# Kernel optimization log

Measured on AMD Instinct MI355X. Metric: run time of the kernel, lower is better.

## Reference

```python
import jax, jax.numpy as jnp
import numpy as np
from jax import lax

CL, IL = 128, 64            # context_length, inst_length (globals in original)
PC, CH1, CH2, CH3 = 64, 128, 256, 256
CK1 = CK2 = CK3 = 3
F1, OUT = 400, 1
B = 4096
C3_OUT = CH3 * (CL - 1 - CK1 - CK2 - CK3 + 3)   # 256*121 = 30976
F1_IN = C3_OUT + CL * IL                        # 39168


def _uni(k, shape, fan_in):
    s = 1.0 / np.sqrt(fan_in)
    return jax.random.uniform(k, shape, jnp.float32, -s, s)


def setup_inputs() -> dict:
    key = jax.random.key(0)
    ks = jax.random.split(key, 14)
    x = jax.random.normal(ks[0], (B, CL * IL), jnp.float32)
    Wp = _uni(ks[1], (PC, IL, 2), IL * 2); bp = _uni(ks[2], (PC,), IL * 2)
    W1 = _uni(ks[3], (CH1, PC, CK1), PC * CK1); b1 = _uni(ks[4], (CH1,), PC * CK1)
    W2 = _uni(ks[5], (CH2, CH1, CK2), CH1 * CK2); b2 = _uni(ks[6], (CH2,), CH1 * CK2)
    W3 = _uni(ks[7], (CH3, CH2, CK3), CH2 * CK3); b3 = _uni(ks[8], (CH3,), CH2 * CK3)
    Wf1 = _uni(ks[9], (F1, F1_IN), F1_IN); bf1 = _uni(ks[10], (F1,), F1_IN)
    Wf2 = _uni(ks[11], (OUT, F1), F1); bf2 = _uni(ks[12], (OUT,), F1)
    return dict(x=x, Wp=Wp, bp=bp, W1=W1, b1=b1, W2=W2, b2=b2,
                W3=W3, b3=b3, Wf1=Wf1, bf1=bf1, Wf2=Wf2, bf2=bf2)


def _conv1d(h, w, b):
    # h: [B,C,L], w: [O,C,K], valid conv, stride 1
    return lax.conv_general_dilated(h, w, (1,), 'VALID',
                                    dimension_numbers=('NCH', 'OIH', 'NCH')) + b[None, :, None]


def reference(x, Wp, bp, W1, b1, W2, b2, W3, b3, Wf1, bf1, Wf2, bf2):
    b = x.shape[0]
    xt = x.reshape(b, CL, IL).transpose(0, 2, 1)          # [B, IL, CL]
    # Fused pairwise convp: original loops i=1..CL-1 over k=2 Conv1d on
    # (x[:,:,0], x[:,:,i]); equivalent to one shared term + one batched matmul.
    base = jnp.einsum('pc,bc->bp', Wp[:, :, 0], xt[:, :, 0])        # [B, PC]
    rest = jnp.einsum('pc,bci->bpi', Wp[:, :, 1], xt[:, :, 1:])     # [B, PC, CL-1]
    h = jax.nn.relu(base[:, :, None] + rest + bp[None, :, None])
    h = jax.nn.relu(_conv1d(h, W1, b1))
    h = jax.nn.relu(_conv1d(h, W2, b2))
    h = jax.nn.relu(_conv1d(h, W3, b3))
    h = h.reshape(b, C3_OUT)
    h = jnp.concatenate([h, xt.reshape(b, IL * CL)], axis=1)        # [B, F1_IN]
    h = jax.nn.relu(h @ Wf1.T + bf1)
    return h @ Wf2.T + bf2
```

## Files before the change

### kernel.cpp

```cpp
#include <hip/hip_runtime.h>


typedef __attribute__((ext_vector_type(8))) short bf16x8;
typedef __attribute__((ext_vector_type(4))) float f32x4;
typedef __attribute__((ext_vector_type(8))) unsigned short u16x8;
typedef __attribute__((ext_vector_type(4))) unsigned short u16x4;

#define DEVINL __device__ __forceinline__

DEVINL unsigned short f2bf(float f) {
  unsigned u = __builtin_bit_cast(unsigned, f);
  return (unsigned short)((u + 0x7fffu + ((u >> 16) & 1u)) >> 16);
}
DEVINL float bf2f(unsigned short h) {
  return __builtin_bit_cast(float, ((unsigned)h) << 16);
}
DEVINL f32x4 mfma16(bf16x8 a, bf16x8 b, f32x4 c) {
  return __builtin_amdgcn_mfma_f32_16x16x32_bf16(a, b, c, 0, 0, 0);
}
DEVINL float relu(float v) { return v > 0.f ? v : 0.f; }
DEVINL int sxg(int r, int c, int sh) {
  return (r << sh) + (((c >> 3) ^ (r & 7)) << 3) + (c & 7);
}

constexpr int NB = 4096;

__global__ __launch_bounds__(256) void k_prep_w(
    const float* __restrict__ Wp, const float* __restrict__ W1,
    const float* __restrict__ W2, const float* __restrict__ W3,
    unsigned short* __restrict__ wp1r, unsigned short* __restrict__ w1p,
    unsigned short* __restrict__ w2p, unsigned short* __restrict__ w3p) {
  int idx = blockIdx.x * 256 + threadIdx.x;
  if (idx < 4096) {
    int p = idx >> 6, i = idx & 63;
    wp1r[idx] = f2bf(Wp[(p * 64 + i) * 2 + 1]);
    return;
  }
  idx -= 4096;
  if (idx < 24576) {
    int f = idx >> 9, l = (idx >> 3) & 63, e = idx & 7;
    int mt = f & 7, t = f >> 3, ks = t & 1, k = t >> 1;
    int o = mt * 16 + (l & 15), c = ks * 32 + (l >> 4) * 8 + e;
    w1p[idx] = f2bf(W1[(o * 64 + c) * 3 + k]);
    return;
  }
  idx -= 24576;
  if (idx < 98304) {
    int f = idx >> 9, l = (idx >> 3) & 63, e = idx & 7;
    int mt = f & 15, t = f >> 4, ks = t & 3, k = t >> 2;
    int o = mt * 16 + (l & 15), c = ks * 32 + (l >> 4) * 8 + e;
    w2p[idx] = f2bf(W2[(o * 128 + c) * 3 + k]);
    return;
  }
  idx -= 98304;
  if (idx < 196608) {
    int f = idx >> 9, l = (idx >> 3) & 63, e = idx & 7;
    int mt = f & 15, t = f >> 4, ks = t & 7, k = t >> 3;
    int o = mt * 16 + (l & 15), c = ks * 32 + (l >> 4) * 8 + e;
    w3p[idx] = f2bf(W3[(o * 256 + c) * 3 + k]);
  }
}

__global__ __launch_bounds__(256) void k_prep_wf1(const float* __restrict__ wf1,
                                                  unsigned short* __restrict__ wf1r) {
  extern __shared__ unsigned short tls[];
  const int m = blockIdx.x, tid = threadIdx.x;
  const float* src = wf1 + (size_t)m * 39168;
  unsigned short* dst = wf1r + (size_t)m * 39168;
  for (int idx = tid; idx < 30976; idx += 256) {
    int o = idx / 121, l = idx - o * 121;
    tls[o * 130 + l] = f2bf(src[idx]);
  }
  __syncthreads();
  for (int idx = tid; idx < 30976; idx += 256) {
    int l = idx >> 8, o = idx & 255;
    dst[idx] = tls[o * 130 + l];
  }
  __syncthreads();
  for (int idx = tid; idx < 8192; idx += 256) {
    int il = idx >> 7, cl = idx & 127;
    tls[cl * 66 + il] = f2bf(src[30976 + idx]);
  }
  __syncthreads();
  for (int idx = tid; idx < 8192; idx += 256) {
    int cl = idx >> 6, il = idx & 63;
    dst[30976 + idx] = tls[cl * 66 + il];
  }
}

template <int CIN, int COUT, int LIN, int LOUT, int SSHI, int SSHO, bool TOGLB>
DEVINL void conv16(const unsigned short* in_lds,
                   const unsigned short* __restrict__ wpack,
                   const float* __restrict__ bias, unsigned short* out_lds,
                   unsigned short* h3, int b, int lane, int wv) {
  constexpr int KS = CIN / 32;
  constexpr int MT = COUT / 16;
  constexpr int MPW = MT / 4;
  const int lr = lane & 15, lq = lane >> 4;
  const int wm = wv >> 1, wn = wv & 1;
  f32x4 acc[MPW][4];
#pragma unroll
  for (int mi = 0; mi < MPW; ++mi)
#pragma unroll
    for (int ni = 0; ni < 4; ++ni) acc[mi][ni] = (f32x4){0.f, 0.f, 0.f, 0.f};
#pragma unroll
  for (int k = 0; k < 3; ++k)
#pragma unroll
    for (int ks = 0; ks < KS; ++ks) {
      bf16x8 a[MPW];
#pragma unroll
      for (int mi = 0; mi < MPW; ++mi)
        a[mi] = *(const bf16x8*)(wpack +
                                 (((k * KS + ks) * MT + wm * MPW + mi) << 9) +
                                 lane * 8);
      const int col = ks * 32 + lq * 8;
#pragma unroll
      for (int ni = 0; ni < 4; ++ni) {
        int l = (wn * 4 + ni) * 16 + lr + k;
        if (l > LIN - 1) l = LIN - 1;
        bf16x8 bb = *(const bf16x8*)(in_lds + sxg(l, col, SSHI));
#pragma unroll
        for (int mi = 0; mi < MPW; ++mi) acc[mi][ni] = mfma16(a[mi], bb, acc[mi][ni]);
      }
    }
#pragma unroll
  for (int mi = 0; mi < MPW; ++mi) {
    const int o0 = (wm * MPW + mi) * 16 + lq * 4;
    const f32x4 bi = *(const f32x4*)(bias + o0);
#pragma unroll
    for (int ni = 0; ni < 4; ++ni) {
      const int l = (wn * 4 + ni) * 16 + lr;
      if (l < LOUT) {
        u16x4 pk;
#pragma unroll
        for (int r = 0; r < 4; ++r) pk[r] = f2bf(relu(acc[mi][ni][r] + bi[r]));
        if constexpr (TOGLB)
          *(u16x4*)(h3 + ((size_t)b * LOUT + l) * COUT + o0) = pk;
        else
          *(u16x4*)(out_lds + sxg(l, o0, SSHO)) = pk;
      }
    }
  }
}

__global__ __launch_bounds__(512) void k_front(
    const float* __restrict__ x, const float* __restrict__ Wp,
    const float* __restrict__ bp, const unsigned short* __restrict__ wp1r,
    const unsigned short* __restrict__ w1p, const float* __restrict__ b1,
    const unsigned short* __restrict__ w2p, const float* __restrict__ b2,
    const unsigned short* __restrict__ w3p, const float* __restrict__ b3,
    unsigned short* __restrict__ h3) {
  extern __shared__ unsigned short lds[];
  unsigned short* xs = lds;
  unsigned short* h1s = lds;
  unsigned short* h0s = lds + 16000;
  unsigned short* h2s = lds + 16000;
  __shared__ float pbase[8][64];
  __shared__ float basel[64];
  const int b = blockIdx.x, tid = threadIdx.x;
  const int lane = tid & 63, wv = tid >> 6, lq = lane >> 4, lr = lane & 15;
  const float* xb = x + (size_t)b * 8192;

  for (int idx = tid * 4; idx < 8192; idx += 2048) {
    f32x4 v = *(const f32x4*)(xb + idx);
    int c = idx >> 6, i = idx & 63;
    u16x4 pk;
#pragma unroll
    for (int r = 0; r < 4; ++r) pk[r] = f2bf(v[r]);
    *(u16x4*)(xs + sxg(c, i, 6)) = pk;
  }
  __syncthreads();

  {
    int p = tid & 63, q = tid >> 6;
    float s = 0.f;
#pragma unroll
    for (int t = 0; t < 8; ++t) {
      int i = q * 8 + t;
      s += Wp[(p * 64 + i) * 2] * bf2f(xs[i]);
    }
    pbase[q][p] = s;
  }
  __syncthreads();
  if (tid < 64) {
    float s = bp[tid];
#pragma unroll
    for (int q = 0; q < 8; ++q) s += pbase[q][tid];
    basel[tid] = s;
  }
  __syncthreads();

  {
    const int mt = wv & 3, nh = wv >> 2;
    f32x4 acc[4];
#pragma unroll
    for (int t = 0; t < 4; ++t) acc[t] = (f32x4){0.f, 0.f, 0.f, 0.f};
#pragma unroll
    for (int s = 0; s < 2; ++s) {
      bf16x8 a = *(const bf16x8*)(wp1r + (mt * 16 + lr) * 64 + s * 32 + lq * 8);
#pragma unroll
      for (int t = 0; t < 4; ++t) {
        int j = (nh * 4 + t) * 16 + lr;
        int row = j + 1 > 127 ? 127 : j + 1;
        bf16x8 bb = *(const bf16x8*)(xs + sxg(row, s * 32 + lq * 8, 6));
        acc[t] = mfma16(a, bb, acc[t]);
      }
    }
    const int m0 = mt * 16 + lq * 4;
    f32x4 bl;
#pragma unroll
    for (int r = 0; r < 4; ++r) bl[r] = basel[m0 + r];
#pragma unroll
    for (int t = 0; t < 4; ++t) {
      int j = (nh * 4 + t) * 16 + lr;
      if (j < 127) {
        u16x4 pk;
#pragma unroll
        for (int r = 0; r < 4; ++r) pk[r] = f2bf(relu(acc[t][r] + bl[r]));
        *(u16x4*)(h0s + sxg(j, m0, 6)) = pk;
      }
    }
  }
  __syncthreads();

  conv16<64, 128, 127, 125, 6, 7, false>(h0s, w1p, b1, h1s, nullptr, b, lane, wv);
  __syncthreads();
  conv16<128, 256, 125, 123, 7, 8, false>(h1s, w2p, b2, h2s, nullptr, b, lane, wv);
  __syncthreads();
  conv16<256, 256, 123, 121, 8, 0, true>(h2s, w3p, b3, nullptr, h3, b, lane, wv);
}

__global__ __launch_bounds__(512) void k_fc1(const unsigned short* __restrict__ h3,
                                             const float* __restrict__ x,
                                             const unsigned short* __restrict__ wf1r,
                                             float* __restrict__ fpart, int chunkN) {
  __shared__ unsigned short lB[128 * 64];
  const int tid = threadIdx.x;
  const int lane = tid & 63, wv = tid >> 6, lq = lane >> 4, lr = lane & 15;
  const int slice = blockIdx.x & 31;
  const int bbase = (blockIdx.x >> 5) * 128;
  const int c0 = slice * 19 + (slice < 4 ? slice : 4);
  const int c1 = c0 + 19 + (slice < 4 ? 1 : 0);

  f32x4 acc[3][8], acc24;
#pragma unroll
  for (int mi = 0; mi < 3; ++mi)
#pragma unroll
    for (int nt = 0; nt < 8; ++nt) acc[mi][nt] = (f32x4){0.f, 0.f, 0.f, 0.f};
  acc24 = (f32x4){0.f, 0.f, 0.f, 0.f};

  const size_t arow0 = (size_t)((3 * wv + 0) * 16 + lr) * 39168;
  const size_t arow1 = (size_t)((3 * wv + 1) * 16 + lr) * 39168;
  const size_t arow2 = (size_t)((3 * wv + 2) * 16 + lr) * 39168;
  const size_t arow24 = (size_t)(384 + lr) * 39168;

  for (int kc = c0; kc < c1; ++kc) {
    const int k0 = kc * 64;
#pragma unroll
    for (int t = 0; t < 2; ++t) {
      int idx = tid + t * 512;
      int n = idx >> 3, ch = idx & 7;
      int bb = bbase + n;
      u16x8 v;
      if (k0 < 30976) {
        v = *(const u16x8*)(h3 + (size_t)bb * 30976 + k0 + ch * 8);
      } else {
        const float* sxp = x + (size_t)bb * 8192 + (k0 - 30976) + ch * 8;
        f32x4 v0 = *(const f32x4*)sxp;
        f32x4 v1 = *(const f32x4*)(sxp + 4);
#pragma unroll
        for (int r = 0; r < 4; ++r) {
          v[r] = f2bf(v0[r]);
          v[4 + r] = f2bf(v1[r]);
        }
      }
      *(u16x8*)(lB + (n << 6) + ((ch ^ (n & 7)) << 3)) = v;
    }
    __syncthreads();

#pragma unroll
    for (int win = 0; win < 2; ++win) {
      const int koff = k0 + win * 32 + lq * 8;
      bf16x8 a0 = *(const bf16x8*)(wf1r + arow0 + koff);
      bf16x8 a1 = *(const bf16x8*)(wf1r + arow1 + koff);
      bf16x8 a2 = *(const bf16x8*)(wf1r + arow2 + koff);
      bf16x8 a24 = *(const bf16x8*)(wf1r + arow24 + koff);
      const int cloc = win * 32 + lq * 8;
#pragma unroll
      for (int nt = 0; nt < 8; ++nt) {
        const int n = nt * 16 + lr;
        bf16x8 bb = *(const bf16x8*)(lB + sxg(n, cloc, 6));
        acc[0][nt] = mfma16(a0, bb, acc[0][nt]);
        acc[1][nt] = mfma16(a1, bb, acc[1][nt]);
        acc[2][nt] = mfma16(a2, bb, acc[2][nt]);
      }
      {
        const int n = wv * 16 + lr;
        bf16x8 bb = *(const bf16x8*)(lB + sxg(n, cloc, 6));
        acc24 = mfma16(a24, bb, acc24);
      }
    }
    __syncthreads();
  }

#pragma unroll
  for (int mi = 0; mi < 3; ++mi) {
    const int m0 = (3 * wv + mi) * 16 + lq * 4;
#pragma unroll
    for (int nt = 0; nt < 8; ++nt) {
      const int bb = bbase + nt * 16 + lr;
      *(f32x4*)(fpart + ((size_t)slice * chunkN + bb) * 400 + m0) = acc[mi][nt];
    }
  }
  {
    const int bb = bbase + wv * 16 + lr;
    *(f32x4*)(fpart + ((size_t)slice * chunkN + bb) * 400 + 384 + lq * 4) = acc24;
  }
}

__global__ __launch_bounds__(256) void k_fc1red(const float* __restrict__ fpart,
                                                const float* __restrict__ bf1,
                                                float* __restrict__ fc, int chunkN) {
  int idx = blockIdx.x * 256 + threadIdx.x;
  if (idx >= chunkN * 400) return;
  int m = idx % 400;
  float s = bf1[m];
  size_t stride = (size_t)chunkN * 400;
#pragma unroll 8
  for (int sl = 0; sl < 32; ++sl) s += fpart[(size_t)sl * stride + idx];
  fc[idx] = relu(s);
}

__global__ __launch_bounds__(256) void k_fc2(const float* __restrict__ fc,
                                             const float* __restrict__ wf2,
                                             const float* __restrict__ bf2,
                                             float* __restrict__ out) {
  int b = blockIdx.x * 4 + (threadIdx.x >> 6);
  int lane = threadIdx.x & 63;
  float s = 0.f;
  for (int m = lane; m < 400; m += 64) s += fc[(size_t)b * 400 + m] * wf2[m];
#pragma unroll
  for (int off = 32; off > 0; off >>= 1) s += __shfl_down(s, off, 64);
  if (lane == 0) out[b] = s + bf2[0];
}

extern "C" void kernel_launch(void* const* d_in, const int* in_sizes, int n_in,
                              void* d_out, int out_size, void* d_ws, size_t ws_size,
                              hipStream_t stream) {
  const float* x = (const float*)d_in[0];
  const float* Wp = (const float*)d_in[1];
  const float* bp = (const float*)d_in[2];
  const float* W1 = (const float*)d_in[3];
  const float* b1 = (const float*)d_in[4];
  const float* W2 = (const float*)d_in[5];
  const float* b2 = (const float*)d_in[6];
  const float* W3 = (const float*)d_in[7];
  const float* b3 = (const float*)d_in[8];
  const float* Wf1 = (const float*)d_in[9];
  const float* bf1 = (const float*)d_in[10];
  const float* Wf2 = (const float*)d_in[11];
  const float* bf2 = (const float*)d_in[12];
  float* out = (float*)d_out;

  static const int cand[4] = {4, 8, 16, 32};
  const size_t fixed = 8192 + 49152 + 196608 + 393216 + 31334400ULL;
  int nchunk = 32;
  for (int i = 0; i < 4; ++i) {
    size_t cn = NB / cand[i];
    size_t need = fixed + cn * 61952ULL + 32ULL * cn * 1600ULL + cn * 1600ULL;
    if (need <= ws_size) {
      nchunk = cand[i];
      break;
    }
  }
  const int chunkN = NB / nchunk;

  char* ws = (char*)d_ws;
  size_t off = 0;
  unsigned short* h3c = (unsigned short*)(ws + off);
  off += (size_t)chunkN * 61952ULL;
  float* fpart = (float*)(ws + off);
  off += 32ULL * chunkN * 1600ULL;
  float* fc = (float*)(ws + off);
  off += (size_t)chunkN * 1600ULL;
  unsigned short* wp1r = (unsigned short*)(ws + off);
  off += 8192;
  unsigned short* w1p = (unsigned short*)(ws + off);
  off += 49152;
  unsigned short* w2p = (unsigned short*)(ws + off);
  off += 196608;
  unsigned short* w3p = (unsigned short*)(ws + off);
  off += 393216;
  unsigned short* wf1r = (unsigned short*)(ws + off);

  k_prep_w<<<1264, 256, 0, stream>>>(Wp, W1, W2, W3, wp1r, w1p, w2p, w3p);
  k_prep_wf1<<<400, 256, 66560, stream>>>(Wf1, wf1r);

  for (int c = 0; c < nchunk; ++c) {
    const float* xc = x + (size_t)c * chunkN * 8192;
    k_front<<<chunkN, 512, 94976, stream>>>(xc, Wp, bp, wp1r, w1p, b1, w2p, b2,
                                            w3p, b3, h3c);
    k_fc1<<<(chunkN / 128) * 32, 512, 0, stream>>>(h3c, xc, wf1r, fpart, chunkN);
    k_fc1red<<<(chunkN * 400 + 255) / 256, 256, 0, stream>>>(fpart, bf1, fc, chunkN);
    k_fc2<<<chunkN / 4, 256, 0, stream>>>(fc, Wf2, bf2, out + (size_t)c * chunkN);
  }
}
```

Measured before the change: 770.6 us.

## Restructure FC1 as register-tiled direct-load GEMM with bf16 x staging and re-tiled convs

The FC1 kernel drops LDS staging and instead loads the bf16 activation and weight fragments straight from global memory into registers. Each block covers a 208-row weight panel against 256 batch rows, and the K split is adaptive so the grid stays at 256 blocks. The weight matrix is zero-padded to 416 rows and the front kernel now writes a bf16 copy of x, so FC1 no longer converts fp32 inputs on the fly. The conv layers are re-tiled so each wave owns more output channels and fewer positions, and the workspace chunk sizing is reworked. In exchange, pressure on the vector registers and cache goes up, and the extra bf16 x buffer adds global write traffic.

```diff
diff --git a/kernel.cpp b/kernel.cpp
--- a/kernel.cpp
+++ b/kernel.cpp
@@ -65,8 +65,12 @@
                                                   unsigned short* __restrict__ wf1r) {
   extern __shared__ unsigned short tls[];
   const int m = blockIdx.x, tid = threadIdx.x;
+  unsigned short* dst = wf1r + (size_t)m * 39168;
+  if (m >= 400) {
+    for (int idx = tid; idx < 39168; idx += 256) dst[idx] = 0;
+    return;
+  }
   const float* src = wf1 + (size_t)m * 39168;
-  unsigned short* dst = wf1r + (size_t)m * 39168;
   for (int idx = tid; idx < 30976; idx += 256) {
     int o = idx / 121, l = idx - o * 121;
     tls[o * 130 + l] = f2bf(src[idx]);
@@ -88,21 +92,24 @@
   }
 }
 
-template <int CIN, int COUT, int LIN, int LOUT, int SSHI, int SSHO, bool TOGLB>
+template <int CIN, int COUT, int LIN, int LOUT, int SSHI, int SSHO, int MPW,
+          int NPW, bool TOGLB>
 DEVINL void conv16(const unsigned short* in_lds,
                    const unsigned short* __restrict__ wpack,
                    const float* __restrict__ bias, unsigned short* out_lds,
                    unsigned short* h3, int b, int lane, int wv) {
   constexpr int KS = CIN / 32;
   constexpr int MT = COUT / 16;
-  constexpr int MPW = MT / 4;
+  constexpr int GM = MT / MPW;
+  constexpr int GN = 8 / GM;
+  static_assert(GN * NPW == 8, "");
   const int lr = lane & 15, lq = lane >> 4;
-  const int wm = wv >> 1, wn = wv & 1;
-  f32x4 acc[MPW][4];
+  const int wm = wv / GN, wn = wv % GN;
+  f32x4 acc[MPW][NPW];
 #pragma unroll
   for (int mi = 0; mi < MPW; ++mi)
 #pragma unroll
-    for (int ni = 0; ni < 4; ++ni) acc[mi][ni] = (f32x4){0.f, 0.f, 0.f, 0.f};
+    for (int ni = 0; ni < NPW; ++ni) acc[mi][ni] = (f32x4){0.f, 0.f, 0.f, 0.f};
 #pragma unroll
   for (int k = 0; k < 3; ++k)
 #pragma unroll
@@ -115,12 +122,13 @@
                                  lane * 8);
       const int col = ks * 32 + lq * 8;
 #pragma unroll
-      for (int ni = 0; ni < 4; ++ni) {
-        int l = (wn * 4 + ni) * 16 + lr + k;
+      for (int ni = 0; ni < NPW; ++ni) {
+        int l = (wn * NPW + ni) * 16 + lr + k;
         if (l > LIN - 1) l = LIN - 1;
         bf16x8 bb = *(const bf16x8*)(in_lds + sxg(l, col, SSHI));
 #pragma unroll
-        for (int mi = 0; mi < MPW; ++mi) acc[mi][ni] = mfma16(a[mi], bb, acc[mi][ni]);
+        for (int mi = 0; mi < MPW; ++mi)
+          acc[mi][ni] = mfma16(a[mi], bb, acc[mi][ni]);
       }
     }
 #pragma unroll
@@ -128,8 +136,8 @@
     const int o0 = (wm * MPW + mi) * 16 + lq * 4;
     const f32x4 bi = *(const f32x4*)(bias + o0);
 #pragma unroll
-    for (int ni = 0; ni < 4; ++ni) {
-      const int l = (wn * 4 + ni) * 16 + lr;
+    for (int ni = 0; ni < NPW; ++ni) {
+      const int l = (wn * NPW + ni) * 16 + lr;
       if (l < LOUT) {
         u16x4 pk;
 #pragma unroll
@@ -149,7 +157,7 @@
     const unsigned short* __restrict__ w1p, const float* __restrict__ b1,
     const unsigned short* __restrict__ w2p, const float* __restrict__ b2,
     const unsigned short* __restrict__ w3p, const float* __restrict__ b3,
-    unsigned short* __restrict__ h3) {
+    unsigned short* __restrict__ h3, unsigned short* __restrict__ xbf) {
   extern __shared__ unsigned short lds[];
   unsigned short* xs = lds;
   unsigned short* h1s = lds;
@@ -168,6 +176,7 @@
 #pragma unroll
     for (int r = 0; r < 4; ++r) pk[r] = f2bf(v[r]);
     *(u16x4*)(xs + sxg(c, i, 6)) = pk;
+    *(u16x4*)(xbf + (size_t)b * 8192 + idx) = pk;
   }
   __syncthreads();
 
@@ -223,111 +232,92 @@
   }
   __syncthreads();
 
-  conv16<64, 128, 127, 125, 6, 7, false>(h0s, w1p, b1, h1s, nullptr, b, lane, wv);
-  __syncthreads();
-  conv16<128, 256, 125, 123, 7, 8, false>(h1s, w2p, b2, h2s, nullptr, b, lane, wv);
-  __syncthreads();
-  conv16<256, 256, 123, 121, 8, 0, true>(h2s, w3p, b3, nullptr, h3, b, lane, wv);
+  conv16<64, 128, 127, 125, 6, 7, 8, 1, false>(h0s, w1p, b1, h1s, nullptr, b,
+                                               lane, wv);
+  __syncthreads();
+  conv16<128, 256, 125, 123, 7, 8, 8, 2, false>(h1s, w2p, b2, h2s, nullptr, b,
+                                                lane, wv);
+  __syncthreads();
+  conv16<256, 256, 123, 121, 8, 0, 8, 2, true>(h2s, w3p, b3, nullptr, h3, b,
+                                               lane, wv);
 }
 
 __global__ __launch_bounds__(512) void k_fc1(const unsigned short* __restrict__ h3,
-                                             const float* __restrict__ x,
+                                             const unsigned short* __restrict__ xbf,
                                              const unsigned short* __restrict__ wf1r,
-                                             float* __restrict__ fpart, int chunkN) {
-  __shared__ unsigned short lB[128 * 64];
+                                             float* __restrict__ fpart, int chunkN,
+                                             int S, int NBC) {
   const int tid = threadIdx.x;
   const int lane = tid & 63, wv = tid >> 6, lq = lane >> 4, lr = lane & 15;
-  const int slice = blockIdx.x & 31;
-  const int bbase = (blockIdx.x >> 5) * 128;
-  const int c0 = slice * 19 + (slice < 4 ? slice : 4);
-  const int c1 = c0 + 19 + (slice < 4 ? 1 : 0);
-
-  f32x4 acc[3][8], acc24;
-#pragma unroll
-  for (int mi = 0; mi < 3; ++mi)
-#pragma unroll
-    for (int nt = 0; nt < 8; ++nt) acc[mi][nt] = (f32x4){0.f, 0.f, 0.f, 0.f};
-  acc24 = (f32x4){0.f, 0.f, 0.f, 0.f};
-
-  const size_t arow0 = (size_t)((3 * wv + 0) * 16 + lr) * 39168;
-  const size_t arow1 = (size_t)((3 * wv + 1) * 16 + lr) * 39168;
-  const size_t arow2 = (size_t)((3 * wv + 2) * 16 + lr) * 39168;
-  const size_t arow24 = (size_t)(384 + lr) * 39168;
-
-  for (int kc = c0; kc < c1; ++kc) {
-    const int k0 = kc * 64;
-#pragma unroll
-    for (int t = 0; t < 2; ++t) {
-      int idx = tid + t * 512;
-      int n = idx >> 3, ch = idx & 7;
-      int bb = bbase + n;
-      u16x8 v;
-      if (k0 < 30976) {
-        v = *(const u16x8*)(h3 + (size_t)bb * 30976 + k0 + ch * 8);
-      } else {
-        const float* sxp = x + (size_t)bb * 8192 + (k0 - 30976) + ch * 8;
-        f32x4 v0 = *(const f32x4*)sxp;
-        f32x4 v1 = *(const f32x4*)(sxp + 4);
-#pragma unroll
-        for (int r = 0; r < 4; ++r) {
-          v[r] = f2bf(v0[r]);
-          v[4 + r] = f2bf(v1[r]);
-        }
-      }
-      *(u16x8*)(lB + (n << 6) + ((ch ^ (n & 7)) << 3)) = v;
-    }
-    __syncthreads();
-
-#pragma unroll
-    for (int win = 0; win < 2; ++win) {
-      const int koff = k0 + win * 32 + lq * 8;
-      bf16x8 a0 = *(const bf16x8*)(wf1r + arow0 + koff);
-      bf16x8 a1 = *(const bf16x8*)(wf1r + arow1 + koff);
-      bf16x8 a2 = *(const bf16x8*)(wf1r + arow2 + koff);
-      bf16x8 a24 = *(const bf16x8*)(wf1r + arow24 + koff);
-      const int cloc = win * 32 + lq * 8;
-#pragma unroll
-      for (int nt = 0; nt < 8; ++nt) {
-        const int n = nt * 16 + lr;
-        bf16x8 bb = *(const bf16x8*)(lB + sxg(n, cloc, 6));
-        acc[0][nt] = mfma16(a0, bb, acc[0][nt]);
-        acc[1][nt] = mfma16(a1, bb, acc[1][nt]);
-        acc[2][nt] = mfma16(a2, bb, acc[2][nt]);
-      }
-      {
-        const int n = wv * 16 + lr;
-        bf16x8 bb = *(const bf16x8*)(lB + sxg(n, cloc, 6));
-        acc24 = mfma16(a24, bb, acc24);
-      }
-    }
-    __syncthreads();
-  }
-
-#pragma unroll
-  for (int mi = 0; mi < 3; ++mi) {
-    const int m0 = (3 * wv + mi) * 16 + lq * 4;
-#pragma unroll
-    for (int nt = 0; nt < 8; ++nt) {
-      const int bb = bbase + nt * 16 + lr;
-      *(f32x4*)(fpart + ((size_t)slice * chunkN + bb) * 400 + m0) = acc[mi][nt];
-    }
-  }
-  {
-    const int bb = bbase + wv * 16 + lr;
-    *(f32x4*)(fpart + ((size_t)slice * chunkN + bb) * 400 + 384 + lq * 4) = acc24;
+  const int x8 = blockIdx.x & 7, r = blockIdx.x >> 3;
+  const int nb = r % NBC, q = r / NBC;
+  const int panel = q * 8 + x8;
+  const int slice = panel >> 1, mh = panel & 1;
+  const int bbase = nb * 256;
+  const int per = 1224 / S, rem = 1224 - per * S;
+  const int c0 = slice * per + (slice < rem ? slice : rem);
+  const int c1 = c0 + per + (slice < rem ? 1 : 0);
+
+  f32x4 acc[13][2];
+#pragma unroll
+  for (int mt = 0; mt < 13; ++mt) {
+    acc[mt][0] = (f32x4){0.f, 0.f, 0.f, 0.f};
+    acc[mt][1] = (f32x4){0.f, 0.f, 0.f, 0.f};
+  }
+
+  size_t arow[13];
+#pragma unroll
+  for (int mt = 0; mt < 13; ++mt)
+    arow[mt] = (size_t)(mh * 208 + mt * 16 + lr) * 39168;
+
+  const int bb0 = bbase + (wv * 2 + 0) * 16 + lr;
+  const int bb1 = bbase + (wv * 2 + 1) * 16 + lr;
+  const unsigned short* pb0h = h3 + (size_t)bb0 * 30976;
+  const unsigned short* pb1h = h3 + (size_t)bb1 * 30976;
+  const unsigned short* pb0x = xbf + (size_t)bb0 * 8192;
+  const unsigned short* pb1x = xbf + (size_t)bb1 * 8192;
+
+#define FC1_BODY(P0, P1, KOFF)                                               \
+  {                                                                          \
+    const int k = kk * 32 + lq * 8;                                          \
+    bf16x8 av[13];                                                           \
+    _Pragma("unroll") for (int mt = 0; mt < 13; ++mt) av[mt] =               \
+        *(const bf16x8*)(wf1r + arow[mt] + k);                               \
+    bf16x8 bbf0 = *(const bf16x8*)((P0) + (k - (KOFF)));                     \
+    bf16x8 bbf1 = *(const bf16x8*)((P1) + (k - (KOFF)));                     \
+    _Pragma("unroll") for (int mt = 0; mt < 13; ++mt) {                      \
+      acc[mt][0] = mfma16(av[mt], bbf0, acc[mt][0]);                         \
+      acc[mt][1] = mfma16(av[mt], bbf1, acc[mt][1]);                         \
+    }                                                                        \
+  }
+
+  const int hb = c1 < 968 ? c1 : 968;
+  for (int kk = c0; kk < hb; ++kk) FC1_BODY(pb0h, pb1h, 0)
+  const int xa = c0 > 968 ? c0 : 968;
+  for (int kk = xa; kk < c1; ++kk) FC1_BODY(pb0x, pb1x, 30976)
+#undef FC1_BODY
+
+#pragma unroll
+  for (int mt = 0; mt < 13; ++mt) {
+    const int m0 = mh * 208 + mt * 16 + lq * 4;
+#pragma unroll
+    for (int ni = 0; ni < 2; ++ni) {
+      const int bb = bbase + (wv * 2 + ni) * 16 + lr;
+      *(f32x4*)(fpart + ((size_t)slice * chunkN + bb) * 416 + m0) = acc[mt][ni];
+    }
   }
 }
 
 __global__ __launch_bounds__(256) void k_fc1red(const float* __restrict__ fpart,
                                                 const float* __restrict__ bf1,
-                                                float* __restrict__ fc, int chunkN) {
+                                                float* __restrict__ fc, int chunkN,
+                                                int S) {
   int idx = blockIdx.x * 256 + threadIdx.x;
   if (idx >= chunkN * 400) return;
-  int m = idx % 400;
+  int bq = idx / 400, m = idx - bq * 400;
   float s = bf1[m];
-  size_t stride = (size_t)chunkN * 400;
-#pragma unroll 8
-  for (int sl = 0; sl < 32; ++sl) s += fpart[(size_t)sl * stride + idx];
+  for (int sl = 0; sl < S; ++sl)
+    s += fpart[((size_t)sl * chunkN + bq) * 416 + m];
   fc[idx] = relu(s);
 }
 
@@ -362,25 +352,32 @@
   const float* bf2 = (const float*)d_in[12];
   float* out = (float*)d_out;
 
-  static const int cand[4] = {4, 8, 16, 32};
-  const size_t fixed = 8192 + 49152 + 196608 + 393216 + 31334400ULL;
-  int nchunk = 32;
-  for (int i = 0; i < 4; ++i) {
-    size_t cn = NB / cand[i];
-    size_t need = fixed + cn * 61952ULL + 32ULL * cn * 1600ULL + cn * 1600ULL;
-    if (need <= ws_size) {
-      nchunk = cand[i];
-      break;
-    }
-  }
-  const int chunkN = NB / nchunk;
+  const size_t fixedw = 8192 + 49152 + 196608 + 393216 + 416ULL * 39168 * 2;
+  const size_t fpartB = 32768ULL * 416 * 4;
+  int chunkN = 512;
+  {
+    const int cands[3] = {2048, 1024, 512};
+    for (int i = 0; i < 3; ++i) {
+      size_t need = fixedw + fpartB +
+                    (size_t)cands[i] * (61952ULL + 16384ULL + 1600ULL);
+      if (need <= ws_size) {
+        chunkN = cands[i];
+        break;
+      }
+    }
+  }
+  const int nchunk = NB / chunkN;
+  const int NBC = chunkN / 256;
+  const int S = 128 / NBC;
 
   char* ws = (char*)d_ws;
   size_t off = 0;
   unsigned short* h3c = (unsigned short*)(ws + off);
   off += (size_t)chunkN * 61952ULL;
+  unsigned short* xbfc = (unsigned short*)(ws + off);
+  off += (size_t)chunkN * 16384ULL;
   float* fpart = (float*)(ws + off);
-  off += 32ULL * chunkN * 1600ULL;
+  off += fpartB;
   float* fc = (float*)(ws + off);
   off += (size_t)chunkN * 1600ULL;
   unsigned short* wp1r = (unsigned short*)(ws + off);
@@ -394,14 +391,15 @@
   unsigned short* wf1r = (unsigned short*)(ws + off);
 
   k_prep_w<<<1264, 256, 0, stream>>>(Wp, W1, W2, W3, wp1r, w1p, w2p, w3p);
-  k_prep_wf1<<<400, 256, 66560, stream>>>(Wf1, wf1r);
+  k_prep_wf1<<<416, 256, 66560, stream>>>(Wf1, wf1r);
 
   for (int c = 0; c < nchunk; ++c) {
     const float* xc = x + (size_t)c * chunkN * 8192;
     k_front<<<chunkN, 512, 94976, stream>>>(xc, Wp, bp, wp1r, w1p, b1, w2p, b2,
-                                            w3p, b3, h3c);
-    k_fc1<<<(chunkN / 128) * 32, 512, 0, stream>>>(h3c, xc, wf1r, fpart, chunkN);
-    k_fc1red<<<(chunkN * 400 + 255) / 256, 256, 0, stream>>>(fpart, bf1, fc, chunkN);
+                                            w3p, b3, h3c, xbfc);
+    k_fc1<<<256, 512, 0, stream>>>(h3c, xbfc, wf1r, fpart, chunkN, S, NBC);
+    k_fc1red<<<(chunkN * 400 + 255) / 256, 256, 0, stream>>>(fpart, bf1, fc,
+                                                             chunkN, S);
     k_fc2<<<chunkN / 4, 256, 0, stream>>>(fc, Wf2, bf2, out + (size_t)c * chunkN);
   }
 }
```

Measured after the change: 1.181 ms. +53.3%, slower.

## Split conv2/conv3 into two row halves to shrink LDS and raise occupancy

Applied to the files above, without the earlier changes.

Conv2 and conv3 in the front kernel now each run in two halves over output rows, reusing a half-size h2 buffer. This cuts dynamic LDS from about 95KB to about 65KB so more blocks can be resident per CU. The cost is extra barriers and recomputing overlapping conv2 rows at the split. The Wp tap-0 weights are also pre-converted to transposed bf16 for coalesced reads, and the Wf1 prep kernel is split across 2000 smaller blocks.

```diff
diff --git a/kernel.cpp b/kernel.cpp
--- a/kernel.cpp
+++ b/kernel.cpp
@@ -28,12 +28,14 @@
 __global__ __launch_bounds__(256) void k_prep_w(
     const float* __restrict__ Wp, const float* __restrict__ W1,
     const float* __restrict__ W2, const float* __restrict__ W3,
-    unsigned short* __restrict__ wp1r, unsigned short* __restrict__ w1p,
-    unsigned short* __restrict__ w2p, unsigned short* __restrict__ w3p) {
+    unsigned short* __restrict__ wp1r, unsigned short* __restrict__ wp0r,
+    unsigned short* __restrict__ w1p, unsigned short* __restrict__ w2p,
+    unsigned short* __restrict__ w3p) {
   int idx = blockIdx.x * 256 + threadIdx.x;
   if (idx < 4096) {
     int p = idx >> 6, i = idx & 63;
-    wp1r[idx] = f2bf(Wp[(p * 64 + i) * 2 + 1]);
+    wp1r[p * 64 + i] = f2bf(Wp[(p * 64 + i) * 2 + 1]);
+    wp0r[i * 64 + p] = f2bf(Wp[(p * 64 + i) * 2 + 0]);
     return;
   }
   idx -= 4096;
@@ -64,45 +66,52 @@
 __global__ __launch_bounds__(256) void k_prep_wf1(const float* __restrict__ wf1,
                                                   unsigned short* __restrict__ wf1r) {
   extern __shared__ unsigned short tls[];
-  const int m = blockIdx.x, tid = threadIdx.x;
-  const float* src = wf1 + (size_t)m * 39168;
+  const int m = blockIdx.x / 5, q = blockIdx.x % 5, tid = threadIdx.x;
   unsigned short* dst = wf1r + (size_t)m * 39168;
-  for (int idx = tid; idx < 30976; idx += 256) {
-    int o = idx / 121, l = idx - o * 121;
-    tls[o * 130 + l] = f2bf(src[idx]);
-  }
-  __syncthreads();
-  for (int idx = tid; idx < 30976; idx += 256) {
-    int l = idx >> 8, o = idx & 255;
-    dst[idx] = tls[o * 130 + l];
-  }
-  __syncthreads();
-  for (int idx = tid; idx < 8192; idx += 256) {
-    int il = idx >> 7, cl = idx & 127;
-    tls[cl * 66 + il] = f2bf(src[30976 + idx]);
-  }
-  __syncthreads();
-  for (int idx = tid; idx < 8192; idx += 256) {
-    int cl = idx >> 6, il = idx & 63;
-    dst[30976 + idx] = tls[cl * 66 + il];
-  }
-}
-
-template <int CIN, int COUT, int LIN, int LOUT, int SSHI, int SSHO, bool TOGLB>
-DEVINL void conv16(const unsigned short* in_lds,
-                   const unsigned short* __restrict__ wpack,
-                   const float* __restrict__ bias, unsigned short* out_lds,
-                   unsigned short* h3, int b, int lane, int wv) {
+  if (q < 4) {
+    const float* src = wf1 + (size_t)m * 39168 + q * 7744;
+    for (int idx = tid; idx < 7744; idx += 256) {
+      int o = idx / 121, l = idx - o * 121;
+      tls[o * 132 + l] = f2bf(src[idx]);
+    }
+    __syncthreads();
+    for (int idx = tid; idx < 7744; idx += 256) {
+      int l = idx >> 6, o = idx & 63;
+      dst[l * 256 + q * 64 + o] = tls[o * 132 + l];
+    }
+  } else {
+    const float* src = wf1 + (size_t)m * 39168 + 30976;
+    for (int idx = tid; idx < 8192; idx += 256) {
+      int il = idx >> 7, cl = idx & 127;
+      tls[cl * 66 + il] = f2bf(src[idx]);
+    }
+    __syncthreads();
+    for (int idx = tid; idx < 8192; idx += 256) {
+      int cl = idx >> 6, il = idx & 63;
+      dst[30976 + idx] = tls[cl * 66 + il];
+    }
+  }
+}
+
+template <int CIN, int COUT, int SSHI, int SSHO, int MPW, int NPW, bool TOGLB>
+DEVINL void conv_phase(const unsigned short* in_lds,
+                       const unsigned short* __restrict__ wpack,
+                       const float* __restrict__ bias,
+                       unsigned short* out_lds, unsigned short* h3, int b,
+                       int lane, int wv, int rowoff, int rowclamp, int outbase,
+                       int outvalid) {
   constexpr int KS = CIN / 32;
   constexpr int MT = COUT / 16;
-  constexpr int MPW = MT / 4;
+  constexpr int GM = MT / MPW;
+  constexpr int GN = 8 / GM;
+  static_assert(GM * GN == 8, "");
   const int lr = lane & 15, lq = lane >> 4;
-  const int wm = wv >> 1, wn = wv & 1;
-  f32x4 acc[MPW][4];
+  const int wm = wv / GN, wn = wv % GN;
+  f32x4 acc[MPW][NPW];
 #pragma unroll
   for (int mi = 0; mi < MPW; ++mi)
 #pragma unroll
-    for (int ni = 0; ni < 4; ++ni) acc[mi][ni] = (f32x4){0.f, 0.f, 0.f, 0.f};
+    for (int ni = 0; ni < NPW; ++ni) acc[mi][ni] = (f32x4){0.f, 0.f, 0.f, 0.f};
 #pragma unroll
   for (int k = 0; k < 3; ++k)
 #pragma unroll
@@ -115,12 +124,13 @@
                                  lane * 8);
       const int col = ks * 32 + lq * 8;
 #pragma unroll
-      for (int ni = 0; ni < 4; ++ni) {
-        int l = (wn * 4 + ni) * 16 + lr + k;
-        if (l > LIN - 1) l = LIN - 1;
-        bf16x8 bb = *(const bf16x8*)(in_lds + sxg(l, col, SSHI));
-#pragma unroll
-        for (int mi = 0; mi < MPW; ++mi) acc[mi][ni] = mfma16(a[mi], bb, acc[mi][ni]);
+      for (int ni = 0; ni < NPW; ++ni) {
+        int row = rowoff + (wn * NPW + ni) * 16 + lr + k;
+        if (row > rowclamp) row = rowclamp;
+        bf16x8 bb = *(const bf16x8*)(in_lds + sxg(row, col, SSHI));
+#pragma unroll
+        for (int mi = 0; mi < MPW; ++mi)
+          acc[mi][ni] = mfma16(a[mi], bb, acc[mi][ni]);
       }
     }
 #pragma unroll
@@ -128,23 +138,23 @@
     const int o0 = (wm * MPW + mi) * 16 + lq * 4;
     const f32x4 bi = *(const f32x4*)(bias + o0);
 #pragma unroll
-    for (int ni = 0; ni < 4; ++ni) {
-      const int l = (wn * 4 + ni) * 16 + lr;
-      if (l < LOUT) {
+    for (int ni = 0; ni < NPW; ++ni) {
+      const int ll = (wn * NPW + ni) * 16 + lr;
+      if (ll < outvalid) {
         u16x4 pk;
 #pragma unroll
         for (int r = 0; r < 4; ++r) pk[r] = f2bf(relu(acc[mi][ni][r] + bi[r]));
         if constexpr (TOGLB)
-          *(u16x4*)(h3 + ((size_t)b * LOUT + l) * COUT + o0) = pk;
+          *(u16x4*)(h3 + ((size_t)b * 121 + outbase + ll) * 256 + o0) = pk;
         else
-          *(u16x4*)(out_lds + sxg(l, o0, SSHO)) = pk;
+          *(u16x4*)(out_lds + sxg(ll, o0, SSHO)) = pk;
       }
     }
   }
 }
 
 __global__ __launch_bounds__(512) void k_front(
-    const float* __restrict__ x, const float* __restrict__ Wp,
+    const float* __restrict__ x, const unsigned short* __restrict__ wp0r,
     const float* __restrict__ bp, const unsigned short* __restrict__ wp1r,
     const unsigned short* __restrict__ w1p, const float* __restrict__ b1,
     const unsigned short* __restrict__ w2p, const float* __restrict__ b2,
@@ -152,9 +162,9 @@
     unsigned short* __restrict__ h3) {
   extern __shared__ unsigned short lds[];
   unsigned short* xs = lds;
-  unsigned short* h1s = lds;
-  unsigned short* h0s = lds + 16000;
-  unsigned short* h2s = lds + 16000;
+  unsigned short* h0s = lds + 8192;
+  unsigned short* h2h = lds;
+  unsigned short* h1s = lds + 16384;
   __shared__ float pbase[8][64];
   __shared__ float basel[64];
   const int b = blockIdx.x, tid = threadIdx.x;
@@ -177,7 +187,7 @@
 #pragma unroll
     for (int t = 0; t < 8; ++t) {
       int i = q * 8 + t;
-      s += Wp[(p * 64 + i) * 2] * bf2f(xs[i]);
+      s += bf2f(wp0r[i * 64 + p]) * bf2f(xs[i]);
     }
     pbase[q][p] = s;
   }
@@ -223,11 +233,20 @@
   }
   __syncthreads();
 
-  conv16<64, 128, 127, 125, 6, 7, false>(h0s, w1p, b1, h1s, nullptr, b, lane, wv);
-  __syncthreads();
-  conv16<128, 256, 125, 123, 7, 8, false>(h1s, w2p, b2, h2s, nullptr, b, lane, wv);
-  __syncthreads();
-  conv16<256, 256, 123, 121, 8, 0, true>(h2s, w3p, b3, nullptr, h3, b, lane, wv);
+  conv_phase<64, 128, 6, 7, 2, 4, false>(h0s, w1p, b1, h1s, nullptr, b, lane,
+                                         wv, 0, 126, 0, 125);
+  __syncthreads();
+  conv_phase<128, 256, 7, 8, 4, 2, false>(h1s, w2p, b2, h2h, nullptr, b, lane,
+                                          wv, 0, 124, 0, 64);
+  __syncthreads();
+  conv_phase<256, 256, 8, 0, 2, 4, true>(h2h, w3p, b3, nullptr, h3, b, lane,
+                                         wv, 0, 63, 0, 62);
+  __syncthreads();
+  conv_phase<128, 256, 7, 8, 4, 2, false>(h1s, w2p, b2, h2h, nullptr, b, lane,
+                                          wv, 62, 124, 0, 61);
+  __syncthreads();
+  conv_phase<256, 256, 8, 0, 2, 4, true>(h2h, w3p, b3, nullptr, h3, b, lane,
+                                         wv, 0, 63, 62, 59);
 }
 
 __global__ __launch_bounds__(512) void k_fc1(const unsigned short* __restrict__ h3,
@@ -362,8 +381,9 @@
   const float* bf2 = (const float*)d_in[12];
   float* out = (float*)d_out;
 
+  const size_t fixed =
+      8192 + 8192 + 49152 + 196608 + 393216 + 400ULL * 39168 * 2;
   static const int cand[4] = {4, 8, 16, 32};
-  const size_t fixed = 8192 + 49152 + 196608 + 393216 + 31334400ULL;
   int nchunk = 32;
   for (int i = 0; i < 4; ++i) {
     size_t cn = NB / cand[i];
@@ -385,6 +405,8 @@
   off += (size_t)chunkN * 1600ULL;
   unsigned short* wp1r = (unsigned short*)(ws + off);
   off += 8192;
+  unsigned short* wp0r = (unsigned short*)(ws + off);
+  off += 8192;
   unsigned short* w1p = (unsigned short*)(ws + off);
   off += 49152;
   unsigned short* w2p = (unsigned short*)(ws + off);
@@ -393,15 +415,16 @@
   off += 393216;
   unsigned short* wf1r = (unsigned short*)(ws + off);
 
-  k_prep_w<<<1264, 256, 0, stream>>>(Wp, W1, W2, W3, wp1r, w1p, w2p, w3p);
-  k_prep_wf1<<<400, 256, 66560, stream>>>(Wf1, wf1r);
+  k_prep_w<<<1264, 256, 0, stream>>>(Wp, W1, W2, W3, wp1r, wp0r, w1p, w2p, w3p);
+  k_prep_wf1<<<2000, 256, 16896, stream>>>(Wf1, wf1r);
 
   for (int c = 0; c < nchunk; ++c) {
     const float* xc = x + (size_t)c * chunkN * 8192;
-    k_front<<<chunkN, 512, 94976, stream>>>(xc, Wp, bp, wp1r, w1p, b1, w2p, b2,
-                                            w3p, b3, h3c);
+    k_front<<<chunkN, 512, 64768, stream>>>(xc, wp0r, bp, wp1r, w1p, b1, w2p,
+                                            b2, w3p, b3, h3c);
     k_fc1<<<(chunkN / 128) * 32, 512, 0, stream>>>(h3c, xc, wf1r, fpart, chunkN);
-    k_fc1red<<<(chunkN * 400 + 255) / 256, 256, 0, stream>>>(fpart, bf1, fc, chunkN);
+    k_fc1red<<<(chunkN * 400 + 255) / 256, 256, 0, stream>>>(fpart, bf1, fc,
+                                                             chunkN);
     k_fc2<<<chunkN / 4, 256, 0, stream>>>(fc, Wf2, bf2, out + (size_t)c * chunkN);
   }
 }
```

Measured after the change: 781.1 us. About the same (+1.4%).
